# Kernel optimization log

Hardware: AMD Instinct MI355X
Metric: run time of the kernel (lower is better)

## Reference

```python
import jax, jax.numpy as jnp
import numpy as np

VOCAB, EMB, HID = 1000, 128, 256
B, T = 64, 1024


def setup_inputs() -> dict:
    key = jax.random.key(0)
    k1, k2, k3, k4, k5, k6, k7 = jax.random.split(key, 7)
    loading_lists = jax.random.randint(k1, (B, T), 0, VOCAB)
    lengths = jnp.maximum(jax.random.randint(k2, (B,), 0, T), 1)  # length >= 1 as in env
    s_ih = 1.0 / np.sqrt(HID)
    return {
        "loading_lists": loading_lists,
        "loading_list_lengths": lengths,
        "emb": jax.random.normal(k3, (VOCAB, EMB), dtype=jnp.float32),
        "W_ih": jax.random.uniform(k4, (4 * HID, EMB), minval=-s_ih, maxval=s_ih, dtype=jnp.float32),
        "W_hh": jax.random.uniform(k5, (4 * HID, HID), minval=-s_ih, maxval=s_ih, dtype=jnp.float32),
        "b_ih": jax.random.uniform(k6, (4 * HID,), minval=-s_ih, maxval=s_ih, dtype=jnp.float32),
        "b_hh": jax.random.uniform(k7, (4 * HID,), minval=-s_ih, maxval=s_ih, dtype=jnp.float32),
    }


def reference(loading_lists, loading_list_lengths, emb, W_ih, W_hh, b_ih, b_hh):
    # Embedding lookup: [B, T, E]
    x = emb[loading_lists]
    Bv, Tv, _ = x.shape
    H = W_hh.shape[1]
    # Precompute input projections for all timesteps: [B, T, 4H]
    xproj = jnp.einsum("bte,ge->btg", x, W_ih) + b_ih + b_hh
    xproj_t = jnp.swapaxes(xproj, 0, 1)  # [T, B, 4H]
    lengths = loading_list_lengths

    def step(carry, inp):
        h, c = carry
        xw_t, t = inp
        gates = xw_t + h @ W_hh.T  # [B, 4H]
        i_g, f_g, g_g, o_g = jnp.split(gates, 4, axis=-1)  # torch gate order i,f,g,o
        i_g = jax.nn.sigmoid(i_g)
        f_g = jax.nn.sigmoid(f_g)
        g_g = jnp.tanh(g_g)
        o_g = jax.nn.sigmoid(o_g)
        c_new = f_g * c + i_g * g_g
        h_new = o_g * jnp.tanh(c_new)
        valid = (t < lengths)[:, None]  # freeze state past each sample's length
        h = jnp.where(valid, h_new, h)
        c = jnp.where(valid, c_new, c)
        return (h, c), None

    h0 = jnp.zeros((Bv, H), dtype=x.dtype)
    c0 = jnp.zeros((Bv, H), dtype=x.dtype)
    (h_last, _), _ = jax.lax.scan(step, (h0, c0), (xproj_t, jnp.arange(Tv)))
    return h_last  # [B, H]
```

## Files before the change

kernel.cpp:

```cpp
#include <hip/hip_runtime.h>
#include <math.h>

#define VOCAB 1000
#define EMB   128
#define HID   256
#define G4    1024
#define BATCH 64
#define SEQT  1024
#define KV    92
#define KL    36

typedef unsigned int u32;
typedef _Float16 f16;
typedef __attribute__((ext_vector_type(2))) _Float16 h2v;
union H2U { u32 u; h2v h; unsigned short s[2]; };

#if defined(__has_builtin)
# if __has_builtin(__builtin_amdgcn_fdot2)
#  define HAVE_FDOT2 1
# endif
#endif
__device__ __forceinline__ float fdot2_(u32 a, u32 b, float c) {
    H2U ua, ub; ua.u = a; ub.u = b;
#ifdef HAVE_FDOT2
    return __builtin_amdgcn_fdot2(ua.h, ub.h, c, false);
#else
    return c + (float)ua.h.x * (float)ub.h.x + (float)ua.h.y * (float)ub.h.y;
#endif
}

__device__ __forceinline__ float sigmoidf_(float x) {
    return 1.f / (1.f + __expf(-x));
}
__device__ __forceinline__ float tanhf_(float x) {
    return 1.f - 2.f / (__expf(2.f * x) + 1.f);
}

__global__ __launch_bounds__(1024) void eproj_kernel(
    const float* __restrict__ emb, const float* __restrict__ W_ih,
    const float* __restrict__ b_ih, const float* __restrict__ b_hh,
    float* __restrict__ eproj)
{
    const int v = blockIdx.x;
    const int g = threadIdx.x;
    __shared__ __align__(16) float x_sh[EMB];
    if (g < EMB / 4) {
        ((float4*)x_sh)[g] = ((const float4*)(emb + (size_t)v * EMB))[g];
    }
    __syncthreads();
    const float4* wrow = (const float4*)(W_ih + (size_t)g * EMB);
    float a0 = 0.f, a1 = 0.f, a2 = 0.f, a3 = 0.f;
#pragma unroll
    for (int e4 = 0; e4 < EMB / 4; e4++) {
        float4 wv = wrow[e4];
        float4 xv = ((const float4*)x_sh)[e4];
        a0 += wv.x * xv.x;
        a1 += wv.y * xv.y;
        a2 += wv.z * xv.z;
        a3 += wv.w * xv.w;
    }
    eproj[(size_t)v * G4 + g] = (a0 + a1) + (a2 + a3) + b_ih[g] + b_hh[g];
}

__global__ __launch_bounds__(128) void pack_whh(
    const float* __restrict__ Whh, u32* __restrict__ wvq, u32* __restrict__ wlq)
{
    const int r = blockIdx.x;
    const int m = threadIdx.x;
    H2U u;
    u.h.x = (f16)Whh[(size_t)r * HID + 2 * m];
    u.h.y = (f16)Whh[(size_t)r * HID + 2 * m + 1];
    if (m < KV) {
        wvq[(size_t)(m >> 2) * (G4 * 4) + r * 4 + (m & 3)] = u.u;
    } else {
        const int mm = m - KV;
        wlq[(size_t)(mm >> 2) * (G4 * 4) + r * 4 + (mm & 3)] = u.u;
    }
}

__global__ __launch_bounds__(512, 2) void lstm_single_cu(
    const int* __restrict__ ids, const int* __restrict__ lens,
    const float* __restrict__ eproj,
    const u32* __restrict__ wvq, const u32* __restrict__ wlq,
    float* __restrict__ out)
{
    const int b   = blockIdx.x;
    const int tau = threadIdx.x;
    const int rA  = tau;
    const int rB  = 512 + tau;

    __shared__ u32 wl_sh[KL / 4 * G4 * 4];
    __shared__ u32 h2_sh[2][HID / 2];
    __shared__ float gs_f[HID], gs_o[HID];

    {
        const uint4* src = (const uint4*)wlq;
        uint4*       dst = (uint4*)wl_sh;
#pragma unroll
        for (int t = 0; t < (KL / 4) * G4 / 512; t++)
            dst[t * 512 + tau] = src[t * 512 + tau];
    }
    if (tau < HID / 2) h2_sh[0][tau] = 0u;

    u32 wA[KV], wB[KV];
#pragma unroll
    for (int q = 0; q < KV / 4; q++) {
        uint4 ta = ((const uint4*)wvq)[q * G4 + rA];
        uint4 tb = ((const uint4*)wvq)[q * G4 + rB];
        wA[4 * q + 0] = ta.x; wA[4 * q + 1] = ta.y;
        wA[4 * q + 2] = ta.z; wA[4 * q + 3] = ta.w;
        wB[4 * q + 0] = tb.x; wB[4 * q + 1] = tb.y;
        wB[4 * q + 2] = tb.z; wB[4 * q + 3] = tb.w;
    }

    const int len = lens[b];
    const int* idr = ids + (size_t)b * SEQT;
    float c = 0.f, hf = 0.f;

    const float* e0 = eproj + (size_t)idr[0] * G4;
    float xA = e0[rA], xB = e0[rB];

    __syncthreads();

    for (int t = 0; t < len; t++) {
        const int nt = (t + 1 < len) ? t + 1 : len - 1;
        const float* en = eproj + (size_t)idr[nt] * G4;
        const float nA = en[rA], nB = en[rB];

        const int p = t & 1;
        const uint4* hb4 = (const uint4*)h2_sh[p];
        float aA = xA, aB = xB;

#pragma unroll
        for (int q = 0; q < KV / 4; q++) {
            uint4 h4 = hb4[q];
            aA = fdot2_(wA[4 * q + 0], h4.x, aA);
            aB = fdot2_(wB[4 * q + 0], h4.x, aB);
            aA = fdot2_(wA[4 * q + 1], h4.y, aA);
            aB = fdot2_(wB[4 * q + 1], h4.y, aB);
            aA = fdot2_(wA[4 * q + 2], h4.z, aA);
            aB = fdot2_(wB[4 * q + 2], h4.z, aB);
            aA = fdot2_(wA[4 * q + 3], h4.w, aA);
            aB = fdot2_(wB[4 * q + 3], h4.w, aB);
        }
#pragma unroll
        for (int q = 0; q < KL / 4; q++) {
            uint4 h4 = hb4[KV / 4 + q];
            uint4 tA = ((const uint4*)wl_sh)[q * G4 + rA];
            uint4 tB = ((const uint4*)wl_sh)[q * G4 + rB];
            aA = fdot2_(tA.x, h4.x, aA);
            aB = fdot2_(tB.x, h4.x, aB);
            aA = fdot2_(tA.y, h4.y, aA);
            aB = fdot2_(tB.y, h4.y, aB);
            aA = fdot2_(tA.z, h4.z, aA);
            aB = fdot2_(tB.z, h4.z, aB);
            aA = fdot2_(tA.w, h4.w, aA);
            aB = fdot2_(tB.w, h4.w, aB);
        }

        if (tau >= HID) {
            gs_f[tau - HID] = aA;
            gs_o[tau - HID] = aB;
        }
        __syncthreads();

        if (tau < HID) {
            float ig = sigmoidf_(aA);
            float gg = tanhf_(aB);
            float fg = sigmoidf_(gs_f[tau]);
            float og = sigmoidf_(gs_o[tau]);
            c = fg * c + ig * gg;
            hf = og * tanhf_(c);
            H2U hv; hv.h.x = (f16)hf; hv.h.y = (f16)0.f;
            ((unsigned short*)h2_sh[p ^ 1])[tau] = hv.s[0];
        }
        xA = nA; xB = nB;
        __syncthreads();
    }

    if (tau < HID) out[(size_t)b * HID + tau] = hf;
}

__global__ __launch_bounds__(1024, 1) void lstm_fallback(
    const int* __restrict__ ids, const int* __restrict__ lens,
    const float* __restrict__ emb, const float* __restrict__ W_ih,
    const float* __restrict__ b_ih, const float* __restrict__ b_hh,
    const float* __restrict__ W_hh, float* __restrict__ out)
{
    const int b = blockIdx.x;
    const int t = threadIdx.x;

    __shared__ __align__(16) float h_sh[HID];
    __shared__ __align__(16) float c_sh[HID];
    __shared__ __align__(16) float gates[G4];
    __shared__ __align__(16) float x_sh[EMB];

    float wih[EMB];
    {
        const float4* wr = (const float4*)(W_ih + (size_t)t * EMB);
#pragma unroll
        for (int e4 = 0; e4 < EMB / 4; e4++) {
            float4 wv = wr[e4];
            wih[4 * e4 + 0] = wv.x;
            wih[4 * e4 + 1] = wv.y;
            wih[4 * e4 + 2] = wv.z;
            wih[4 * e4 + 3] = wv.w;
        }
    }
    float bias = b_ih[t] + b_hh[t];

    const int len = lens[b];
    const int* ids_row = ids + (size_t)b * SEQT;
    if (t < HID) { h_sh[t] = 0.f; c_sh[t] = 0.f; }
    __syncthreads();

    for (int step = 0; step < len; step++) {
        int id = ids_row[step];
        if (t < EMB / 4) {
            ((float4*)x_sh)[t] = ((const float4*)(emb + (size_t)id * EMB))[t];
        }
        __syncthreads();
        float a0 = bias, a1 = 0.f, a2 = 0.f, a3 = 0.f;
#pragma unroll
        for (int e4 = 0; e4 < EMB / 4; e4++) {
            float4 xv = ((const float4*)x_sh)[e4];
            a0 += wih[4 * e4 + 0] * xv.x;
            a1 += wih[4 * e4 + 1] * xv.y;
            a2 += wih[4 * e4 + 2] * xv.z;
            a3 += wih[4 * e4 + 3] * xv.w;
        }
        float acc = (a0 + a1) + (a2 + a3);

        const float* wrow = W_hh + (size_t)t * HID;
        a0 = acc; a1 = 0.f; a2 = 0.f; a3 = 0.f;
        for (int k4 = 0; k4 < HID / 4; k4++) {
            float4 hv = ((const float4*)h_sh)[k4];
            float4 wv = ((const float4*)wrow)[k4];
            a0 += wv.x * hv.x;
            a1 += wv.y * hv.y;
            a2 += wv.z * hv.z;
            a3 += wv.w * hv.w;
        }
        gates[t] = (a0 + a1) + (a2 + a3);
        __syncthreads();

        if (t < HID) {
            float ig = sigmoidf_(gates[t]);
            float fg = sigmoidf_(gates[HID + t]);
            float gg = tanhf_(gates[2 * HID + t]);
            float og = sigmoidf_(gates[3 * HID + t]);
            float cc = fg * c_sh[t] + ig * gg;
            c_sh[t] = cc;
            h_sh[t] = og * tanhf_(cc);
        }
        __syncthreads();
    }
    if (t < HID) out[(size_t)b * HID + t] = h_sh[t];
}

extern "C" void kernel_launch(void* const* d_in, const int* in_sizes, int n_in,
                              void* d_out, int out_size, void* d_ws, size_t ws_size,
                              hipStream_t stream) {
    const int*   ids  = (const int*)d_in[0];
    const int*   lens = (const int*)d_in[1];
    const float* emb  = (const float*)d_in[2];
    const float* Wih  = (const float*)d_in[3];
    const float* Whh  = (const float*)d_in[4];
    const float* bih  = (const float*)d_in[5];
    const float* bhh  = (const float*)d_in[6];
    float* out = (float*)d_out;

    const size_t ep_bytes = (size_t)VOCAB * G4 * sizeof(float);
    const size_t wv_off   = ep_bytes;
    const size_t wv_bytes = (size_t)(KV / 4) * G4 * 4 * sizeof(u32);
    const size_t wl_off   = wv_off + wv_bytes;
    const size_t wl_bytes = (size_t)(KL / 4) * G4 * 4 * sizeof(u32);

    if (ws_size >= wl_off + wl_bytes) {
        float* eproj = (float*)d_ws;
        u32*   wvp   = (u32*)((char*)d_ws + wv_off);
        u32*   wlp   = (u32*)((char*)d_ws + wl_off);
        eproj_kernel<<<VOCAB, 1024, 0, stream>>>(emb, Wih, bih, bhh, eproj);
        pack_whh<<<G4, 128, 0, stream>>>(Whh, wvp, wlp);
        lstm_single_cu<<<BATCH, 512, 0, stream>>>(ids, lens, eproj, wvp, wlp, out);
    } else {
        lstm_fallback<<<BATCH, 1024, 0, stream>>>(
            ids, lens, emb, Wih, bih, bhh, Whh, out);
    }
}
```

Baseline: 1.766 ms.

## Pair gate rows across adjacent lanes and exchange via shuffle, removing mid-step barrier

Each adjacent pair of lanes now holds all four gate rows (i,g in one lane, f,o in the other) for one hidden unit. The gate exchange uses __shfl_xor, so the shared gs_f/gs_o buffers and one __syncthreads per timestep go away. All 512 threads do the cell update work split across even lanes. The weight packing is rearranged per-thread to match, and the h and LDS weight loads are software-prefetched one chunk ahead. This costs some extra register pressure, and half the lanes sit idle during the activation math.

```diff
diff --git a/kernel.cpp b/kernel.cpp
--- a/kernel.cpp
+++ b/kernel.cpp
@@ -7,8 +7,9 @@
 #define G4    1024
 #define BATCH 64
 #define SEQT  1024
-#define KV    92
-#define KL    36
+#define NT    512
+#define KVC   23
+#define KLC   9
 
 typedef unsigned int u32;
 typedef _Float16 f16;
@@ -36,6 +37,14 @@
     return 1.f - 2.f / (__expf(2.f * x) + 1.f);
 }
 
+__device__ __forceinline__ void rows_of(int tau, int& rA, int& rB, int& u, int& e) {
+    const int w = tau >> 6, l = tau & 63;
+    e = l & 1;
+    u = (w << 5) + (l >> 1);
+    rA = e ? (HID + u) : u;
+    rB = e ? (3 * HID + u) : (2 * HID + u);
+}
+
 __global__ __launch_bounds__(1024) void eproj_kernel(
     const float* __restrict__ emb, const float* __restrict__ W_ih,
     const float* __restrict__ b_ih, const float* __restrict__ b_hh,
@@ -62,51 +71,58 @@
     eproj[(size_t)v * G4 + g] = (a0 + a1) + (a2 + a3) + b_ih[g] + b_hh[g];
 }
 
-__global__ __launch_bounds__(128) void pack_whh(
-    const float* __restrict__ Whh, u32* __restrict__ wvq, u32* __restrict__ wlq)
+__global__ __launch_bounds__(NT) void pack_whh(
+    const float* __restrict__ Whh, uint4* __restrict__ wvq, uint4* __restrict__ wlq)
 {
-    const int r = blockIdx.x;
-    const int m = threadIdx.x;
-    H2U u;
-    u.h.x = (f16)Whh[(size_t)r * HID + 2 * m];
-    u.h.y = (f16)Whh[(size_t)r * HID + 2 * m + 1];
-    if (m < KV) {
-        wvq[(size_t)(m >> 2) * (G4 * 4) + r * 4 + (m & 3)] = u.u;
-    } else {
-        const int mm = m - KV;
-        wlq[(size_t)(mm >> 2) * (G4 * 4) + r * 4 + (mm & 3)] = u.u;
-    }
-}
-
-__global__ __launch_bounds__(512, 2) void lstm_single_cu(
+    const int c   = blockIdx.x;
+    const int tau = threadIdx.x;
+    int rA, rB, u, e;
+    rows_of(tau, rA, rB, u, e);
+    const int rows[2] = { rA, rB };
+#pragma unroll
+    for (int slot = 0; slot < 2; slot++) {
+        const int r = rows[slot];
+        const int mbase = 4 * c;
+        const int mc = (c < KVC) ? mbase : (4 * KVC + 4 * (c - KVC));
+        H2U q0, q1, q2, q3;
+        q0.h.x = (f16)Whh[(size_t)r * HID + 2 * (mc + 0)];
+        q0.h.y = (f16)Whh[(size_t)r * HID + 2 * (mc + 0) + 1];
+        q1.h.x = (f16)Whh[(size_t)r * HID + 2 * (mc + 1)];
+        q1.h.y = (f16)Whh[(size_t)r * HID + 2 * (mc + 1) + 1];
+        q2.h.x = (f16)Whh[(size_t)r * HID + 2 * (mc + 2)];
+        q2.h.y = (f16)Whh[(size_t)r * HID + 2 * (mc + 2) + 1];
+        q3.h.x = (f16)Whh[(size_t)r * HID + 2 * (mc + 3)];
+        q3.h.y = (f16)Whh[(size_t)r * HID + 2 * (mc + 3) + 1];
+        uint4 pk = { q0.u, q1.u, q2.u, q3.u };
+        if (c < KVC) wvq[((size_t)c * 2 + slot) * NT + tau] = pk;
+        else         wlq[((size_t)(c - KVC) * 2 + slot) * NT + tau] = pk;
+    }
+}
+
+__global__ __launch_bounds__(NT, 2) void lstm_single_cu(
     const int* __restrict__ ids, const int* __restrict__ lens,
     const float* __restrict__ eproj,
-    const u32* __restrict__ wvq, const u32* __restrict__ wlq,
+    const uint4* __restrict__ wvq, const uint4* __restrict__ wlq,
     float* __restrict__ out)
 {
     const int b   = blockIdx.x;
     const int tau = threadIdx.x;
-    const int rA  = tau;
-    const int rB  = 512 + tau;
-
-    __shared__ u32 wl_sh[KL / 4 * G4 * 4];
-    __shared__ u32 h2_sh[2][HID / 2];
-    __shared__ float gs_f[HID], gs_o[HID];
-
-    {
-        const uint4* src = (const uint4*)wlq;
-        uint4*       dst = (uint4*)wl_sh;
-#pragma unroll
-        for (int t = 0; t < (KL / 4) * G4 / 512; t++)
-            dst[t * 512 + tau] = src[t * 512 + tau];
-    }
+    int rA, rB, u, e;
+    rows_of(tau, rA, rB, u, e);
+
+    __shared__ uint4 wl_sh[KLC * 2 * NT];
+    __shared__ u32   h2_sh[2][HID / 2];
+
+#pragma unroll
+    for (int t = 0; t < (KLC * 2 * NT) / NT; t++)
+        wl_sh[t * NT + tau] = wlq[t * NT + tau];
     if (tau < HID / 2) h2_sh[0][tau] = 0u;
 
-    u32 wA[KV], wB[KV];
-#pragma unroll
-    for (int q = 0; q < KV / 4; q++) {
-        uint4 ta = ((const uint4*)wvq)[q * G4 + rA];
-        uint4 tb = ((const uint4*)wvq)[q * G4 + rB];
+    u32 wA[KVC * 4], wB[KVC * 4];
+#pragma unroll
+    for (int q = 0; q < KVC; q++) {
+        uint4 ta = wvq[(q * 2 + 0) * NT + tau];
+        uint4 tb = wvq[(q * 2 + 1) * NT + tau];
         wA[4 * q + 0] = ta.x; wA[4 * q + 1] = ta.y;
         wA[4 * q + 2] = ta.z; wA[4 * q + 3] = ta.w;
         wB[4 * q + 0] = tb.x; wB[4 * q + 1] = tb.y;
@@ -131,54 +147,59 @@
         const uint4* hb4 = (const uint4*)h2_sh[p];
         float aA = xA, aB = xB;
 
-#pragma unroll
-        for (int q = 0; q < KV / 4; q++) {
-            uint4 h4 = hb4[q];
-            aA = fdot2_(wA[4 * q + 0], h4.x, aA);
-            aB = fdot2_(wB[4 * q + 0], h4.x, aB);
-            aA = fdot2_(wA[4 * q + 1], h4.y, aA);
-            aB = fdot2_(wB[4 * q + 1], h4.y, aB);
-            aA = fdot2_(wA[4 * q + 2], h4.z, aA);
-            aB = fdot2_(wB[4 * q + 2], h4.z, aB);
-            aA = fdot2_(wA[4 * q + 3], h4.w, aA);
-            aB = fdot2_(wB[4 * q + 3], h4.w, aB);
-        }
-#pragma unroll
-        for (int q = 0; q < KL / 4; q++) {
-            uint4 h4 = hb4[KV / 4 + q];
-            uint4 tA = ((const uint4*)wl_sh)[q * G4 + rA];
-            uint4 tB = ((const uint4*)wl_sh)[q * G4 + rB];
-            aA = fdot2_(tA.x, h4.x, aA);
-            aB = fdot2_(tB.x, h4.x, aB);
-            aA = fdot2_(tA.y, h4.y, aA);
-            aB = fdot2_(tB.y, h4.y, aB);
-            aA = fdot2_(tA.z, h4.z, aA);
-            aB = fdot2_(tB.z, h4.z, aB);
-            aA = fdot2_(tA.w, h4.w, aA);
-            aB = fdot2_(tB.w, h4.w, aB);
-        }
-
-        if (tau >= HID) {
-            gs_f[tau - HID] = aA;
-            gs_o[tau - HID] = aB;
-        }
-        __syncthreads();
-
-        if (tau < HID) {
+        uint4 hc = hb4[0];
+#pragma unroll
+        for (int q = 0; q < KVC; q++) {
+            const uint4 hn = hb4[q + 1];
+            aA = fdot2_(wA[4 * q + 0], hc.x, aA);
+            aB = fdot2_(wB[4 * q + 0], hc.x, aB);
+            aA = fdot2_(wA[4 * q + 1], hc.y, aA);
+            aB = fdot2_(wB[4 * q + 1], hc.y, aB);
+            aA = fdot2_(wA[4 * q + 2], hc.z, aA);
+            aB = fdot2_(wB[4 * q + 2], hc.z, aB);
+            aA = fdot2_(wA[4 * q + 3], hc.w, aA);
+            aB = fdot2_(wB[4 * q + 3], hc.w, aB);
+            hc = hn;
+        }
+        uint4 tA = wl_sh[0 * NT + tau];
+        uint4 tB = wl_sh[1 * NT + tau];
+#pragma unroll
+        for (int q = 0; q < KLC; q++) {
+            uint4 tAn, tBn, hn;
+            if (q + 1 < KLC) {
+                tAn = wl_sh[((q + 1) * 2 + 0) * NT + tau];
+                tBn = wl_sh[((q + 1) * 2 + 1) * NT + tau];
+                hn  = hb4[KVC + q + 1];
+            }
+            aA = fdot2_(tA.x, hc.x, aA);
+            aB = fdot2_(tB.x, hc.x, aB);
+            aA = fdot2_(tA.y, hc.y, aA);
+            aB = fdot2_(tB.y, hc.y, aB);
+            aA = fdot2_(tA.z, hc.z, aA);
+            aB = fdot2_(tB.z, hc.z, aB);
+            aA = fdot2_(tA.w, hc.w, aA);
+            aB = fdot2_(tB.w, hc.w, aB);
+            if (q + 1 < KLC) { tA = tAn; tB = tBn; hc = hn; }
+        }
+
+        const float pA = __shfl_xor(aA, 1);
+        const float pB = __shfl_xor(aB, 1);
+
+        if (e == 0) {
             float ig = sigmoidf_(aA);
             float gg = tanhf_(aB);
-            float fg = sigmoidf_(gs_f[tau]);
-            float og = sigmoidf_(gs_o[tau]);
+            float fg = sigmoidf_(pA);
+            float og = sigmoidf_(pB);
             c = fg * c + ig * gg;
             hf = og * tanhf_(c);
             H2U hv; hv.h.x = (f16)hf; hv.h.y = (f16)0.f;
-            ((unsigned short*)h2_sh[p ^ 1])[tau] = hv.s[0];
+            ((unsigned short*)h2_sh[p ^ 1])[u] = hv.s[0];
         }
         xA = nA; xB = nB;
         __syncthreads();
     }
 
-    if (tau < HID) out[(size_t)b * HID + tau] = hf;
+    if (e == 0) out[(size_t)b * HID + u] = hf;
 }
 
 __global__ __launch_bounds__(1024, 1) void lstm_fallback(
@@ -272,17 +293,17 @@
 
     const size_t ep_bytes = (size_t)VOCAB * G4 * sizeof(float);
     const size_t wv_off   = ep_bytes;
-    const size_t wv_bytes = (size_t)(KV / 4) * G4 * 4 * sizeof(u32);
+    const size_t wv_bytes = (size_t)KVC * 2 * NT * sizeof(uint4);
     const size_t wl_off   = wv_off + wv_bytes;
-    const size_t wl_bytes = (size_t)(KL / 4) * G4 * 4 * sizeof(u32);
+    const size_t wl_bytes = (size_t)KLC * 2 * NT * sizeof(uint4);
 
     if (ws_size >= wl_off + wl_bytes) {
         float* eproj = (float*)d_ws;
-        u32*   wvp   = (u32*)((char*)d_ws + wv_off);
-        u32*   wlp   = (u32*)((char*)d_ws + wl_off);
+        uint4* wvp   = (uint4*)((char*)d_ws + wv_off);
+        uint4* wlp   = (uint4*)((char*)d_ws + wl_off);
         eproj_kernel<<<VOCAB, 1024, 0, stream>>>(emb, Wih, bih, bhh, eproj);
-        pack_whh<<<G4, 128, 0, stream>>>(Whh, wvp, wlp);
-        lstm_single_cu<<<BATCH, 512, 0, stream>>>(ids, lens, eproj, wvp, wlp, out);
+        pack_whh<<<KVC + KLC, NT, 0, stream>>>(Whh, wvp, wlp);
+        lstm_single_cu<<<BATCH, NT, 0, stream>>>(ids, lens, eproj, wvp, wlp, out);
     } else {
         lstm_fallback<<<BATCH, 1024, 0, stream>>>(
             ids, lens, emb, Wih, bih, bhh, Whh, out);
```

New measurement: 1.837 ms. 4.0% more time.
